# Kernel tuning notes

Measured on AMD Instinct MI355X. Metric: run time of the kernel, lower is better.

Reference implementation:

```python
import jax, jax.numpy as jnp
import numpy as np

D_MODEL = 1024
D_FF = 4096
NUM_EXPERTS = 8
TOP_K = 2
LB_COEF = 0.01
Z_COEF = 0.001
EPS_LN = 1e-5


def setup_inputs() -> dict:
    key = jax.random.key(0)
    ks = jax.random.split(key, 8)
    B, L = 4, 2048
    s_in = 1.0 / np.sqrt(D_MODEL)
    s_ff = 1.0 / np.sqrt(D_FF)
    return {
        "x": jax.random.normal(ks[0], (B, L, D_MODEL), dtype=jnp.float32),
        "gate_w": jax.random.normal(ks[1], (NUM_EXPERTS, D_MODEL), dtype=jnp.float32) * s_in,
        "ln_g": jnp.ones((D_MODEL,), dtype=jnp.float32),
        "ln_b": jnp.zeros((D_MODEL,), dtype=jnp.float32),
        "w1": jax.random.normal(ks[2], (NUM_EXPERTS, D_MODEL, D_FF), dtype=jnp.float32) * s_in,
        "b1": jnp.zeros((NUM_EXPERTS, D_FF), dtype=jnp.float32),
        "w2": jax.random.normal(ks[3], (NUM_EXPERTS, D_FF, D_MODEL), dtype=jnp.float32) * s_ff,
        "b2": jnp.zeros((NUM_EXPERTS, D_MODEL), dtype=jnp.float32),
    }


def reference(x, gate_w, ln_g, ln_b, w1, b1, w2, b2):
    B, L, D = x.shape
    xf = x.reshape(-1, D)  # [T, D]

    # LayerNorm
    mu = jnp.mean(xf, axis=-1, keepdims=True)
    var = jnp.mean((xf - mu) ** 2, axis=-1, keepdims=True)
    x_norm = (xf - mu) * jax.lax.rsqrt(var + EPS_LN) * ln_g + ln_b

    # Router (eval mode: no noise)
    logits = jnp.clip(x_norm @ gate_w.T, -10.0, 10.0)  # [T, E]
    z_loss = jnp.mean(jax.nn.logsumexp(logits, axis=-1) ** 2) * Z_COEF
    probs = jax.nn.softmax(logits, axis=-1)

    gw, idx = jax.lax.top_k(probs, TOP_K)  # [T, K]
    gw = gw / (jnp.sum(gw, axis=-1, keepdims=True) + 1e-8)

    # Load-balancing aux loss uses top-1 assignment
    top1_mask = jax.nn.one_hot(idx[:, 0], NUM_EXPERTS, dtype=jnp.float32)
    fraction_routed = jnp.mean(top1_mask, axis=0)
    mean_prob = jnp.mean(probs, axis=0)
    aux_loss = NUM_EXPERTS * jnp.sum(fraction_routed * mean_prob) * LB_COEF
    total_aux = aux_loss + z_loss

    # Combine weights [T, E]: sum over k of gate weight where routed to e
    combine = jnp.einsum("tk,tke->te", gw, jax.nn.one_hot(idx, NUM_EXPERTS, dtype=gw.dtype))

    # Dense per-expert FFN (Expert: Linear -> GELU -> Linear), combined by weights
    out = jnp.zeros_like(xf)
    for e in range(NUM_EXPERTS):
        h = jax.nn.gelu(x_norm @ w1[e] + b1[e], approximate=False)
        y = h @ w2[e] + b2[e]
        out = out + combine[:, e:e + 1] * y

    return x + out.reshape(B, L, D), total_aux
```

## Files before the change

kernel.cpp:

```cpp
#include <hip/hip_runtime.h>
#include <math.h>

typedef __bf16 bf16_t;
typedef bf16_t bf16x8 __attribute__((ext_vector_type(8)));
typedef bf16_t bf16x4 __attribute__((ext_vector_type(4)));
typedef float  f32x4  __attribute__((ext_vector_type(4)));

#define T_TOK 8192
#define DM 1024
#define DF 4096
#define NE 8
#define NP 16384

__device__ __forceinline__ f32x4 mfma_bf16(bf16x8 a, bf16x8 b, f32x4 c) {
  return __builtin_amdgcn_mfma_f32_16x16x32_bf16(a, b, c, 0, 0, 0);
}

__device__ __forceinline__ void gload16(const void* g, void* l) {
  __builtin_amdgcn_global_load_lds((const __attribute__((address_space(1))) void*)g,
                                   (__attribute__((address_space(3))) void*)l, 16, 0, 0);
}

__device__ __forceinline__ float erf_fast(float x) {
  float ax = fabsf(x);
  float t = 1.f / (1.f + 0.3275911f * ax);
  float p = t * (0.254829592f + t * (-0.284496736f + t * (1.421413741f +
            t * (-1.453152027f + t * 1.061405429f))));
  float r = 1.f - p * __expf(-ax * ax);
  return copysignf(r, x);
}

__device__ __forceinline__ unsigned swz_off(int row, int ch) {
  return (unsigned)(((row >> 1) << 7) + (((((row & 1) << 2) | ch) ^ ((row >> 1) & 7)) << 4));
}


__global__ __launch_bounds__(256) void k_router(
    const float* __restrict__ x, const float* __restrict__ gate_w,
    const float* __restrict__ ln_g, const float* __restrict__ ln_b,
    float* __restrict__ out, bf16_t* __restrict__ xn,
    int* __restrict__ eidx, float* __restrict__ gts, int* __restrict__ meta)
{
  int* cnt1 = meta;
  int* cnt2 = meta + 8;
  float* probsum = (float*)(meta + 32);
  float* zsum    = (float*)(meta + 40);

  __shared__ float sprob[8];
  __shared__ float sz;
  __shared__ int sc1[8], sc2[8];
  if (threadIdx.x < 8) { sprob[threadIdx.x] = 0.f; sc1[threadIdx.x] = 0; sc2[threadIdx.x] = 0; }
  if (threadIdx.x == 8) sz = 0.f;
  __syncthreads();

  int lane = threadIdx.x & 63, wv = threadIdx.x >> 6;
  int t = blockIdx.x * 4 + wv;
  const float* xt = x + (size_t)t * DM;

  float4 v[4];
  float s1 = 0.f, s2 = 0.f;
  #pragma unroll
  for (int c = 0; c < 4; ++c) {
    v[c] = *(const float4*)(xt + c * 256 + lane * 4);
    s1 += v[c].x + v[c].y + v[c].z + v[c].w;
    s2 += v[c].x * v[c].x + v[c].y * v[c].y + v[c].z * v[c].z + v[c].w * v[c].w;
  }
  #pragma unroll
  for (int o = 32; o > 0; o >>= 1) { s1 += __shfl_xor(s1, o, 64); s2 += __shfl_xor(s2, o, 64); }
  float mu = s1 * (1.f / DM);
  float var = s2 * (1.f / DM) - mu * mu;
  float rstd = rsqrtf(var + 1e-5f);

  float xv[16];
  #pragma unroll
  for (int c = 0; c < 4; ++c) {
    int d = c * 256 + lane * 4;
    float4 g4 = *(const float4*)(ln_g + d);
    float4 b4 = *(const float4*)(ln_b + d);
    xv[c*4+0] = (v[c].x - mu) * rstd * g4.x + b4.x;
    xv[c*4+1] = (v[c].y - mu) * rstd * g4.y + b4.y;
    xv[c*4+2] = (v[c].z - mu) * rstd * g4.z + b4.z;
    xv[c*4+3] = (v[c].w - mu) * rstd * g4.w + b4.w;
    *(float4*)(out + (size_t)t * DM + d) = v[c];
    bf16x4 pk = { (bf16_t)xv[c*4+0], (bf16_t)xv[c*4+1], (bf16_t)xv[c*4+2], (bf16_t)xv[c*4+3] };
    *(bf16x4*)(xn + (size_t)t * DM + d) = pk;
  }

  float lg[8];
  #pragma unroll
  for (int e = 0; e < 8; ++e) {
    float p = 0.f;
    #pragma unroll
    for (int c = 0; c < 4; ++c) {
      int d = c * 256 + lane * 4;
      float4 g4 = *(const float4*)(gate_w + e * DM + d);
      p += xv[c*4+0] * g4.x + xv[c*4+1] * g4.y + xv[c*4+2] * g4.z + xv[c*4+3] * g4.w;
    }
    #pragma unroll
    for (int o = 32; o > 0; o >>= 1) p += __shfl_xor(p, o, 64);
    lg[e] = p;
  }

  if (lane == 0) {
    float m = -1e30f;
    #pragma unroll
    for (int e = 0; e < 8; ++e) { lg[e] = fminf(fmaxf(lg[e], -10.f), 10.f); m = fmaxf(m, lg[e]); }
    float pr[8]; float se = 0.f;
    #pragma unroll
    for (int e = 0; e < 8; ++e) { pr[e] = expf(lg[e] - m); se += pr[e]; }
    float inv = 1.f / se;
    #pragma unroll
    for (int e = 0; e < 8; ++e) pr[e] *= inv;
    float lse = m + logf(se);

    int e0 = 0; float p0 = pr[0];
    #pragma unroll
    for (int e = 1; e < 8; ++e) if (pr[e] > p0) { p0 = pr[e]; e0 = e; }
    int e1 = -1; float p1 = -1.f;
    #pragma unroll
    for (int e = 0; e < 8; ++e) if (e != e0 && pr[e] > p1) { p1 = pr[e]; e1 = e; }
    float s = p0 + p1 + 1e-8f;
    eidx[t*2]   = e0; eidx[t*2+1] = e1;
    gts[t*2]    = p0 / s; gts[t*2+1] = p1 / s;

    atomicAdd(&sc1[e0], 1);
    atomicAdd(&sc2[e0], 1);
    atomicAdd(&sc2[e1], 1);
    #pragma unroll
    for (int e = 0; e < 8; ++e) atomicAdd(&sprob[e], pr[e]);
    atomicAdd(&sz, lse * lse);
  }
  __syncthreads();
  if (threadIdx.x < 8) {
    if (sc1[threadIdx.x]) atomicAdd(&cnt1[threadIdx.x], sc1[threadIdx.x]);
    if (sc2[threadIdx.x]) atomicAdd(&cnt2[threadIdx.x], sc2[threadIdx.x]);
    atomicAdd(&probsum[threadIdx.x], sprob[threadIdx.x]);
  }
  if (threadIdx.x == 8) atomicAdd(zsum, sz);
}

__global__ __launch_bounds__(256) void k_convT2(
    const float* __restrict__ w1, bf16_t* __restrict__ w1t,
    const float* __restrict__ w2, bf16_t* __restrict__ w2t)
{
  int bid = blockIdx.x;
  const float* s; bf16_t* d; int R, C, c0, r0;
  if (bid < 8192) {
    int e = bid >> 10, rem = bid & 1023;
    R = DM; C = DF;
    s = w1 + (size_t)e * R * C; d = w1t + (size_t)e * R * C;
    c0 = (rem & 63) * 64; r0 = (rem >> 6) * 64;
  } else {
    int e = (bid - 8192) >> 10, rem = (bid - 8192) & 1023;
    R = DF; C = DM;
    s = w2 + (size_t)e * R * C; d = w2t + (size_t)e * R * C;
    c0 = (rem & 15) * 64; r0 = (rem >> 4) * 64;
  }

  __shared__ float tile[64][65];
  int t = threadIdx.x;
  #pragma unroll
  for (int i = 0; i < 4; ++i) {
    int idx = i * 256 + t;
    int r = idx >> 4, c4 = (idx & 15) * 4;
    float4 v = *(const float4*)(s + (size_t)(r0 + r) * C + c0 + c4);
    tile[r][c4]   = v.x; tile[r][c4+1] = v.y;
    tile[r][c4+2] = v.z; tile[r][c4+3] = v.w;
  }
  __syncthreads();
  #pragma unroll
  for (int i = 0; i < 2; ++i) {
    int idx = i * 256 + t;
    int c = idx >> 3, r8 = (idx & 7) * 8;
    bf16x8 pk;
    #pragma unroll
    for (int k = 0; k < 8; ++k) pk[k] = (bf16_t)tile[r8 + k][c];
    *(bf16x8*)(d + (size_t)(c0 + c) * R + r0 + r8) = pk;
  }
}

__global__ void k_finalize(int* __restrict__ meta, float* __restrict__ aux_out) {
  if (threadIdx.x == 0 && blockIdx.x == 0) {
    int acc = 0;
    for (int e = 0; e < 8; ++e) { meta[24 + e] = acc; acc += meta[8 + e]; }
    const float* probsum = (const float*)(meta + 32);
    const float* zsum    = (const float*)(meta + 40);
    float s = 0.f;
    for (int e = 0; e < 8; ++e)
      s += ((float)meta[e] * (1.f / 8192.f)) * (probsum[e] * (1.f / 8192.f));
    aux_out[0] = 8.f * s * 0.01f + (zsum[0] * (1.f / 8192.f)) * 0.001f;
  }
}

__global__ __launch_bounds__(256) void k_assign(
    const int* __restrict__ eidx, float* __restrict__ gts,
    int* __restrict__ meta, int* __restrict__ list, float* __restrict__ gl,
    int* __restrict__ t2s)
{
  int t = blockIdx.x * 256 + threadIdx.x;
  int* cursor = meta + 16;
  const int* off = meta + 24;
  #pragma unroll
  for (int k = 0; k < 2; ++k) {
    int e = eidx[t*2 + k];
    float g = gts[t*2 + k];
    int pos = atomicAdd(&cursor[e], 1);
    int slot = off[e] + pos;
    list[slot] = t;
    gl[slot] = g;
    t2s[t*2 + k] = slot;
  }
}


#define STAGE1(KT, BO) do { \
  _Pragma("unroll") for (int r = 0; r < 2; ++r) gload16(sA[r] + (KT) * 32, smem + (BO) + dA[r]); \
  _Pragma("unroll") for (int r = 0; r < 4; ++r) gload16(sB[r] + (KT) * 32, smem + (BO) + dB[r]); \
} while (0)

#define COMPUTE1(BO) do { \
  bf16x8 bfr[4]; \
  _Pragma("unroll") for (int j = 0; j < 4; ++j) bfr[j] = *(const bf16x8*)(smem + (BO) + b_off[j]); \
  _Pragma("unroll") for (int i = 0; i < 8; ++i) { \
    bf16x8 af = *(const bf16x8*)(smem + (BO) + a_off[i]); \
    _Pragma("unroll") for (int j = 0; j < 4; ++j) acc[i][j] = mfma_bf16(af, bfr[j], acc[i][j]); \
  } \
} while (0)

#define WAITV6 do { __builtin_amdgcn_sched_barrier(0); \
  asm volatile("s_waitcnt vmcnt(6)" ::: "memory"); \
  __builtin_amdgcn_sched_barrier(0); __builtin_amdgcn_s_barrier(); \
  __builtin_amdgcn_sched_barrier(0); } while (0)

#define WAITV0 do { __builtin_amdgcn_sched_barrier(0); \
  asm volatile("s_waitcnt vmcnt(0)" ::: "memory"); \
  __builtin_amdgcn_sched_barrier(0); __builtin_amdgcn_s_barrier(); \
  __builtin_amdgcn_sched_barrier(0); } while (0)

#define ENDBAR do { __builtin_amdgcn_sched_barrier(0); \
  __builtin_amdgcn_s_barrier(); __builtin_amdgcn_sched_barrier(0); } while (0)

#define KLOOP(NT) do { \
  STAGE1(0, 0); \
  for (int kt = 0; kt < (NT); kt += 2) { \
    STAGE1(kt + 1, 24576); \
    WAITV6; \
    __builtin_amdgcn_s_setprio(1); \
    COMPUTE1(0); \
    __builtin_amdgcn_s_setprio(0); \
    ENDBAR; \
    if (kt + 2 < (NT)) { STAGE1(kt + 2, 0); WAITV6; } else { WAITV0; } \
    __builtin_amdgcn_s_setprio(1); \
    COMPUTE1(24576); \
    __builtin_amdgcn_s_setprio(0); \
    ENDBAR; \
  } \
} while (0)

__global__ __launch_bounds__(256, 2) void k_ffn1(
    const bf16_t* __restrict__ xn, const bf16_t* __restrict__ w1t,
    const float* __restrict__ b1, bf16_t* __restrict__ H,
    const int* __restrict__ list, const int* __restrict__ meta)
{
  int e = blockIdx.z;
  int cnt = meta[8 + e];
  int m0 = blockIdx.y * 128;
  if (m0 >= cnt) return;
  int offe = meta[24 + e];
  int n0 = blockIdx.x * 256;

  __shared__ __align__(1024) char smem[49152];
  int tid = threadIdx.x, lane = tid & 63, wv = tid >> 6;

  const bf16_t* sA[2]; const bf16_t* sB[4];
  unsigned dA[2], dB[4];
  #pragma unroll
  for (int i = 0; i < 2; ++i) {
    int s = i * 256 + tid;
    int line = s >> 3, u = s & 7, w = u ^ (line & 7);
    int row = (line << 1) | (w >> 2), ch = w & 3;
    int mrow = min(m0 + row, cnt - 1);
    int token = list[offe + mrow];
    sA[i] = xn + (size_t)token * DM + ch * 8;
    dA[i] = (unsigned)(i * 4096 + wv * 1024);
  }
  #pragma unroll
  for (int i = 0; i < 4; ++i) {
    int s = i * 256 + tid;
    int line = s >> 3, u = s & 7, w = u ^ (line & 7);
    int row = (line << 1) | (w >> 2), ch = w & 3;
    sB[i] = w1t + ((size_t)e * DF + n0 + row) * DM + ch * 8;
    dB[i] = (unsigned)(8192 + i * 4096 + wv * 1024);
  }

  unsigned a_off[8], b_off[4];
  #pragma unroll
  for (int i = 0; i < 8; ++i) a_off[i] = swz_off(i * 16 + (lane & 15), lane >> 4);
  #pragma unroll
  for (int j = 0; j < 4; ++j) b_off[j] = 8192u + swz_off(wv * 64 + j * 16 + (lane & 15), lane >> 4);

  f32x4 acc[8][4];
  #pragma unroll
  for (int i = 0; i < 8; ++i)
    #pragma unroll
    for (int j = 0; j < 4; ++j)
      acc[i][j] = (f32x4){0.f, 0.f, 0.f, 0.f};

  KLOOP(DM / 32);

  int rq = (lane >> 4) << 2;
  int cbase = n0 + wv * 64 + (lane & 15);
  #pragma unroll
  for (int i = 0; i < 8; ++i) {
    #pragma unroll
    for (int q = 0; q < 4; ++q) {
      int mg = m0 + i * 16 + rq + q;
      if (mg < cnt) {
        size_t hrow = (size_t)(offe + mg) * DF;
        #pragma unroll
        for (int j = 0; j < 4; ++j) {
          int col = cbase + j * 16;
          float hv = acc[i][j][q] + b1[e * DF + col];
          hv = 0.5f * hv * (1.f + erf_fast(hv * 0.70710678118f));
          H[hrow + col] = (bf16_t)hv;
        }
      }
    }
  }
}

__global__ __launch_bounds__(256, 2) void k_ffn2(
    const bf16_t* __restrict__ H, const bf16_t* __restrict__ w2t,
    const float* __restrict__ b2, bf16_t* __restrict__ Y,
    const int* __restrict__ meta)
{
  int e = blockIdx.z;
  int cnt = meta[8 + e];
  int m0 = blockIdx.y * 128;
  if (m0 >= cnt) return;
  int offe = meta[24 + e];
  int n0 = blockIdx.x * 256;

  __shared__ __align__(1024) char smem[49152];
  int tid = threadIdx.x, lane = tid & 63, wv = tid >> 6;

  const bf16_t* sA[2]; const bf16_t* sB[4];
  unsigned dA[2], dB[4];
  #pragma unroll
  for (int i = 0; i < 2; ++i) {
    int s = i * 256 + tid;
    int line = s >> 3, u = s & 7, w = u ^ (line & 7);
    int row = (line << 1) | (w >> 2), ch = w & 3;
    int mrow = min(m0 + row, cnt - 1);
    sA[i] = H + (size_t)(offe + mrow) * DF + ch * 8;
    dA[i] = (unsigned)(i * 4096 + wv * 1024);
  }
  #pragma unroll
  for (int i = 0; i < 4; ++i) {
    int s = i * 256 + tid;
    int line = s >> 3, u = s & 7, w = u ^ (line & 7);
    int row = (line << 1) | (w >> 2), ch = w & 3;
    sB[i] = w2t + ((size_t)e * DM + n0 + row) * DF + ch * 8;
    dB[i] = (unsigned)(8192 + i * 4096 + wv * 1024);
  }

  unsigned a_off[8], b_off[4];
  #pragma unroll
  for (int i = 0; i < 8; ++i) a_off[i] = swz_off(i * 16 + (lane & 15), lane >> 4);
  #pragma unroll
  for (int j = 0; j < 4; ++j) b_off[j] = 8192u + swz_off(wv * 64 + j * 16 + (lane & 15), lane >> 4);

  f32x4 acc[8][4];
  #pragma unroll
  for (int i = 0; i < 8; ++i)
    #pragma unroll
    for (int j = 0; j < 4; ++j)
      acc[i][j] = (f32x4){0.f, 0.f, 0.f, 0.f};

  KLOOP(DF / 32);

  int rq = (lane >> 4) << 2;
  int cbase = n0 + wv * 64 + (lane & 15);
  #pragma unroll
  for (int i = 0; i < 8; ++i) {
    #pragma unroll
    for (int q = 0; q < 4; ++q) {
      int mg = m0 + i * 16 + rq + q;
      if (mg < cnt) {
        size_t yrow = (size_t)(offe + mg) * DM;
        #pragma unroll
        for (int j = 0; j < 4; ++j) {
          int col = cbase + j * 16;
          Y[yrow + col] = (bf16_t)(acc[i][j][q] + b2[e * DM + col]);
        }
      }
    }
  }
}

__global__ __launch_bounds__(256) void k_combine(
    const bf16_t* __restrict__ Y, const int* __restrict__ t2s,
    const float* __restrict__ gl, float* __restrict__ out)
{
  int lane = threadIdx.x & 63, wv = threadIdx.x >> 6;
  int t = blockIdx.x * 4 + wv;
  int s0 = t2s[t*2], s1 = t2s[t*2 + 1];
  float g0 = gl[s0], g1 = gl[s1];
  const bf16_t* y0 = Y + (size_t)s0 * DM;
  const bf16_t* y1 = Y + (size_t)s1 * DM;
  float* o = out + (size_t)t * DM;
  #pragma unroll
  for (int c = 0; c < 4; ++c) {
    int d = c * 256 + lane * 4;
    float4 r  = *(const float4*)(o + d);
    bf16x4 a = *(const bf16x4*)(y0 + d);
    bf16x4 b = *(const bf16x4*)(y1 + d);
    r.x += g0 * (float)a[0] + g1 * (float)b[0];
    r.y += g0 * (float)a[1] + g1 * (float)b[1];
    r.z += g0 * (float)a[2] + g1 * (float)b[2];
    r.w += g0 * (float)a[3] + g1 * (float)b[3];
    *(float4*)(o + d) = r;
  }
}

extern "C" void kernel_launch(void* const* d_in, const int* in_sizes, int n_in,
                              void* d_out, int out_size, void* d_ws, size_t ws_size,
                              hipStream_t stream) {
  const float* x      = (const float*)d_in[0];
  const float* gate_w = (const float*)d_in[1];
  const float* ln_g   = (const float*)d_in[2];
  const float* ln_b   = (const float*)d_in[3];
  const float* w1     = (const float*)d_in[4];
  const float* b1     = (const float*)d_in[5];
  const float* w2     = (const float*)d_in[6];
  const float* b2     = (const float*)d_in[7];
  float* out = (float*)d_out;

  char* ws = (char*)d_ws;
  bf16_t* xn   = (bf16_t*)(ws);
  bf16_t* w1t  = (bf16_t*)(ws + 16777216ull);
  bf16_t* Y    = (bf16_t*)(ws + 16777216ull);
  bf16_t* w2t  = (bf16_t*)(ws + 83886080ull);
  bf16_t* H    = (bf16_t*)(ws + 150994944ull);
  int*    list = (int*)   (ws + 285212672ull);
  float*  gl   = (float*) (ws + 285278208ull);
  int*    eidx = (int*)   (ws + 285343744ull);
  float*  gts  = (float*) (ws + 285409280ull);
  int*    t2s  = (int*)   (ws + 285409280ull);
  int*    meta = (int*)   (ws + 285474816ull);

  hipMemsetAsync(meta, 0, 256, stream);
  k_router<<<T_TOK / 4, 256, 0, stream>>>(x, gate_w, ln_g, ln_b, out, xn, eidx, gts, meta);
  k_convT2<<<16384, 256, 0, stream>>>(w1, w1t, w2, w2t);
  k_finalize<<<1, 1, 0, stream>>>(meta, out + (size_t)T_TOK * DM);
  k_assign<<<T_TOK / 256, 256, 0, stream>>>(eidx, gts, meta, list, gl, t2s);
  k_ffn1<<<dim3(DF / 256, 64, NE), 256, 0, stream>>>(xn, w1t, b1, H, list, meta);
  k_ffn2<<<dim3(DM / 256, 64, NE), 256, 0, stream>>>(H, w2t, b2, Y, meta);
  k_combine<<<T_TOK / 4, 256, 0, stream>>>(Y, t2s, gl, out);
}
```

Measured before the change: 685.5 us.

## Use 256x256 tiles with 8 waves and a deeper LDS-pipelined GEMM

Both expert FFN GEMMs switch from 128x256 tiles with 4 waves to 256x256 tiles with 8 waves (a 2x4 wave grid). They use 128KB of dynamic LDS holding two buffers of BK=64 split into 32-wide halves. The k-loop is rewritten so global-to-LDS loads for future tiles are interleaved with half-tile MFMA phases, with finer waits and barriers. The aim is better operand reuse per loaded byte and more latency hiding. In exchange, occupancy drops to one block per CU, the grid has fewer blocks, and there are more barriers.

```diff
diff --git a/kernel.cpp b/kernel.cpp
--- a/kernel.cpp
+++ b/kernel.cpp
@@ -213,91 +213,91 @@
 }
 
 
-#define STAGE1(KT, BO) do { \
-  _Pragma("unroll") for (int r = 0; r < 2; ++r) gload16(sA[r] + (KT) * 32, smem + (BO) + dA[r]); \
-  _Pragma("unroll") for (int r = 0; r < 4; ++r) gload16(sB[r] + (KT) * 32, smem + (BO) + dB[r]); \
+#define PBAR do { __builtin_amdgcn_sched_barrier(0); __builtin_amdgcn_s_barrier(); \
+                  __builtin_amdgcn_sched_barrier(0); } while (0)
+#define VWAIT10 do { __builtin_amdgcn_sched_barrier(0); \
+  asm volatile("s_waitcnt vmcnt(10)" ::: "memory"); \
+  __builtin_amdgcn_sched_barrier(0); } while (0)
+#define VWAIT0 do { __builtin_amdgcn_sched_barrier(0); \
+  asm volatile("s_waitcnt vmcnt(0)" ::: "memory"); \
+  __builtin_amdgcn_sched_barrier(0); } while (0)
+
+#define STG_A(T, KS, P) do { \
+  gload16(sAq[0] + (T)*64 + (KS)*32, smem + (P)*65536 + (KS)*16384 + dq[0]); \
+  gload16(sAq[1] + (T)*64 + (KS)*32, smem + (P)*65536 + (KS)*16384 + dq[1]); } while (0)
+#define STG_B(T, KS, P) do { \
+  gload16(sBq[0] + (T)*64 + (KS)*32, smem + (P)*65536 + 32768 + (KS)*16384 + dq[0]); \
+  gload16(sBq[1] + (T)*64 + (KS)*32, smem + (P)*65536 + 32768 + (KS)*16384 + dq[1]); } while (0)
+#define LDA(P, KS) do { _Pragma("unroll") for (int i_ = 0; i_ < 8; ++i_) \
+  afr[i_] = *(const bf16x8*)(smem + (P)*65536 + (KS)*16384 + a_off[i_]); } while (0)
+#define LDB(P, KS, NH) do { \
+  bfr0 = *(const bf16x8*)(smem + (P)*65536 + 32768 + (KS)*16384 + b_off[(NH)*2+0]); \
+  bfr1 = *(const bf16x8*)(smem + (P)*65536 + 32768 + (KS)*16384 + b_off[(NH)*2+1]); } while (0)
+#define FMA(NH) do { __builtin_amdgcn_s_setprio(1); \
+  _Pragma("unroll") for (int i_ = 0; i_ < 8; ++i_) { \
+    acc[i_][(NH)*2+0] = mfma_bf16(afr[i_], bfr0, acc[i_][(NH)*2+0]); \
+    acc[i_][(NH)*2+1] = mfma_bf16(afr[i_], bfr1, acc[i_][(NH)*2+1]); } \
+  __builtin_amdgcn_s_setprio(0); } while (0)
+
+#define TILE_MAIN(T, P) do { \
+  LDA(P,0); LDB(P,0,0); STG_B((T)+1, 1, (P)^1); PBAR; FMA(0); PBAR; \
+  LDB(P,0,1); STG_A((T)+2, 0, P); VWAIT10; PBAR; FMA(1); PBAR; \
+  LDA(P,1); LDB(P,1,0); STG_B((T)+2, 0, P); PBAR; FMA(0); PBAR; \
+  LDB(P,1,1); STG_A((T)+2, 1, P); VWAIT10; PBAR; FMA(1); PBAR; } while (0)
+
+#define GEMM_PIPE(NT) do { \
+  STG_A(0,0,0); STG_B(0,0,0); STG_A(0,1,0); STG_B(0,1,0); \
+  STG_A(1,0,1); STG_B(1,0,1); STG_A(1,1,1); \
+  VWAIT10; PBAR; \
+  for (int t_ = 0; t_ < (NT) - 2; t_ += 2) { TILE_MAIN(t_, 0); TILE_MAIN(t_ + 1, 1); } \
+   \
+  LDA(0,0); LDB(0,0,0); STG_B((NT)-1, 1, 1); PBAR; FMA(0); PBAR; \
+  LDB(0,0,1); VWAIT0; PBAR; FMA(1); PBAR; \
+  LDA(0,1); LDB(0,1,0); PBAR; FMA(0); PBAR; \
+  LDB(0,1,1); PBAR; FMA(1); PBAR; \
+   \
+  LDA(1,0); LDB(1,0,0); PBAR; FMA(0); PBAR; \
+  LDB(1,0,1); PBAR; FMA(1); PBAR; \
+  LDA(1,1); LDB(1,1,0); PBAR; FMA(0); PBAR; \
+  LDB(1,1,1); PBAR; FMA(1); \
 } while (0)
 
-#define COMPUTE1(BO) do { \
-  bf16x8 bfr[4]; \
-  _Pragma("unroll") for (int j = 0; j < 4; ++j) bfr[j] = *(const bf16x8*)(smem + (BO) + b_off[j]); \
-  _Pragma("unroll") for (int i = 0; i < 8; ++i) { \
-    bf16x8 af = *(const bf16x8*)(smem + (BO) + a_off[i]); \
-    _Pragma("unroll") for (int j = 0; j < 4; ++j) acc[i][j] = mfma_bf16(af, bfr[j], acc[i][j]); \
-  } \
-} while (0)
-
-#define WAITV6 do { __builtin_amdgcn_sched_barrier(0); \
-  asm volatile("s_waitcnt vmcnt(6)" ::: "memory"); \
-  __builtin_amdgcn_sched_barrier(0); __builtin_amdgcn_s_barrier(); \
-  __builtin_amdgcn_sched_barrier(0); } while (0)
-
-#define WAITV0 do { __builtin_amdgcn_sched_barrier(0); \
-  asm volatile("s_waitcnt vmcnt(0)" ::: "memory"); \
-  __builtin_amdgcn_sched_barrier(0); __builtin_amdgcn_s_barrier(); \
-  __builtin_amdgcn_sched_barrier(0); } while (0)
-
-#define ENDBAR do { __builtin_amdgcn_sched_barrier(0); \
-  __builtin_amdgcn_s_barrier(); __builtin_amdgcn_sched_barrier(0); } while (0)
-
-#define KLOOP(NT) do { \
-  STAGE1(0, 0); \
-  for (int kt = 0; kt < (NT); kt += 2) { \
-    STAGE1(kt + 1, 24576); \
-    WAITV6; \
-    __builtin_amdgcn_s_setprio(1); \
-    COMPUTE1(0); \
-    __builtin_amdgcn_s_setprio(0); \
-    ENDBAR; \
-    if (kt + 2 < (NT)) { STAGE1(kt + 2, 0); WAITV6; } else { WAITV0; } \
-    __builtin_amdgcn_s_setprio(1); \
-    COMPUTE1(24576); \
-    __builtin_amdgcn_s_setprio(0); \
-    ENDBAR; \
-  } \
-} while (0)
-
-__global__ __launch_bounds__(256, 2) void k_ffn1(
+__global__ __launch_bounds__(512, 1) void k_ffn1(
     const bf16_t* __restrict__ xn, const bf16_t* __restrict__ w1t,
     const float* __restrict__ b1, bf16_t* __restrict__ H,
     const int* __restrict__ list, const int* __restrict__ meta)
 {
+  extern __shared__ char smem[];
   int e = blockIdx.z;
   int cnt = meta[8 + e];
-  int m0 = blockIdx.y * 128;
+  int m0 = blockIdx.y * 256;
   if (m0 >= cnt) return;
   int offe = meta[24 + e];
   int n0 = blockIdx.x * 256;
 
-  __shared__ __align__(1024) char smem[49152];
   int tid = threadIdx.x, lane = tid & 63, wv = tid >> 6;
-
-  const bf16_t* sA[2]; const bf16_t* sB[4];
-  unsigned dA[2], dB[4];
+  int wm = wv >> 2, wn = wv & 3;
+
+  const bf16_t* sAq[2]; const bf16_t* sBq[2];
+  unsigned dq[2];
   #pragma unroll
   for (int i = 0; i < 2; ++i) {
-    int s = i * 256 + tid;
+    int s = i * 512 + tid;
     int line = s >> 3, u = s & 7, w = u ^ (line & 7);
     int row = (line << 1) | (w >> 2), ch = w & 3;
     int mrow = min(m0 + row, cnt - 1);
     int token = list[offe + mrow];
-    sA[i] = xn + (size_t)token * DM + ch * 8;
-    dA[i] = (unsigned)(i * 4096 + wv * 1024);
-  }
-  #pragma unroll
-  for (int i = 0; i < 4; ++i) {
-    int s = i * 256 + tid;
-    int line = s >> 3, u = s & 7, w = u ^ (line & 7);
-    int row = (line << 1) | (w >> 2), ch = w & 3;
-    sB[i] = w1t + ((size_t)e * DF + n0 + row) * DM + ch * 8;
-    dB[i] = (unsigned)(8192 + i * 4096 + wv * 1024);
+    sAq[i] = xn + (size_t)token * DM + ch * 8;
+    sBq[i] = w1t + ((size_t)e * DF + n0 + row) * DM + ch * 8;
+    dq[i] = (unsigned)(i * 8192 + wv * 1024);
   }
 
   unsigned a_off[8], b_off[4];
   #pragma unroll
-  for (int i = 0; i < 8; ++i) a_off[i] = swz_off(i * 16 + (lane & 15), lane >> 4);
-  #pragma unroll
-  for (int j = 0; j < 4; ++j) b_off[j] = 8192u + swz_off(wv * 64 + j * 16 + (lane & 15), lane >> 4);
+  for (int i = 0; i < 8; ++i) a_off[i] = swz_off(wm * 128 + i * 16 + (lane & 15), lane >> 4);
+  #pragma unroll
+  for (int j = 0; j < 4; ++j)
+    b_off[j] = swz_off(wn * 64 + (j >> 1) * 32 + (j & 1) * 16 + (lane & 15), lane >> 4);
 
   f32x4 acc[8][4];
   #pragma unroll
@@ -305,21 +305,22 @@
     #pragma unroll
     for (int j = 0; j < 4; ++j)
       acc[i][j] = (f32x4){0.f, 0.f, 0.f, 0.f};
-
-  KLOOP(DM / 32);
+  bf16x8 afr[8], bfr0, bfr1;
+
+  GEMM_PIPE(DM / 64);
 
   int rq = (lane >> 4) << 2;
-  int cbase = n0 + wv * 64 + (lane & 15);
+  int cb = n0 + wn * 64 + (lane & 15);
   #pragma unroll
   for (int i = 0; i < 8; ++i) {
     #pragma unroll
     for (int q = 0; q < 4; ++q) {
-      int mg = m0 + i * 16 + rq + q;
+      int mg = m0 + wm * 128 + i * 16 + rq + q;
       if (mg < cnt) {
         size_t hrow = (size_t)(offe + mg) * DF;
         #pragma unroll
         for (int j = 0; j < 4; ++j) {
-          int col = cbase + j * 16;
+          int col = cb + (j >> 1) * 32 + (j & 1) * 16;
           float hv = acc[i][j][q] + b1[e * DF + col];
           hv = 0.5f * hv * (1.f + erf_fast(hv * 0.70710678118f));
           H[hrow + col] = (bf16_t)hv;
@@ -329,46 +330,41 @@
   }
 }
 
-__global__ __launch_bounds__(256, 2) void k_ffn2(
+__global__ __launch_bounds__(512, 1) void k_ffn2(
     const bf16_t* __restrict__ H, const bf16_t* __restrict__ w2t,
     const float* __restrict__ b2, bf16_t* __restrict__ Y,
     const int* __restrict__ meta)
 {
+  extern __shared__ char smem[];
   int e = blockIdx.z;
   int cnt = meta[8 + e];
-  int m0 = blockIdx.y * 128;
+  int m0 = blockIdx.y * 256;
   if (m0 >= cnt) return;
   int offe = meta[24 + e];
   int n0 = blockIdx.x * 256;
 
-  __shared__ __align__(1024) char smem[49152];
   int tid = threadIdx.x, lane = tid & 63, wv = tid >> 6;
-
-  const bf16_t* sA[2]; const bf16_t* sB[4];
-  unsigned dA[2], dB[4];
+  int wm = wv >> 2, wn = wv & 3;
+
+  const bf16_t* sAq[2]; const bf16_t* sBq[2];
+  unsigned dq[2];
   #pragma unroll
   for (int i = 0; i < 2; ++i) {
-    int s = i * 256 + tid;
+    int s = i * 512 + tid;
     int line = s >> 3, u = s & 7, w = u ^ (line & 7);
     int row = (line << 1) | (w >> 2), ch = w & 3;
     int mrow = min(m0 + row, cnt - 1);
-    sA[i] = H + (size_t)(offe + mrow) * DF + ch * 8;
-    dA[i] = (unsigned)(i * 4096 + wv * 1024);
-  }
-  #pragma unroll
-  for (int i = 0; i < 4; ++i) {
-    int s = i * 256 + tid;
-    int line = s >> 3, u = s & 7, w = u ^ (line & 7);
-    int row = (line << 1) | (w >> 2), ch = w & 3;
-    sB[i] = w2t + ((size_t)e * DM + n0 + row) * DF + ch * 8;
-    dB[i] = (unsigned)(8192 + i * 4096 + wv * 1024);
+    sAq[i] = H + (size_t)(offe + mrow) * DF + ch * 8;
+    sBq[i] = w2t + ((size_t)e * DM + n0 + row) * DF + ch * 8;
+    dq[i] = (unsigned)(i * 8192 + wv * 1024);
   }
 
   unsigned a_off[8], b_off[4];
   #pragma unroll
-  for (int i = 0; i < 8; ++i) a_off[i] = swz_off(i * 16 + (lane & 15), lane >> 4);
-  #pragma unroll
-  for (int j = 0; j < 4; ++j) b_off[j] = 8192u + swz_off(wv * 64 + j * 16 + (lane & 15), lane >> 4);
+  for (int i = 0; i < 8; ++i) a_off[i] = swz_off(wm * 128 + i * 16 + (lane & 15), lane >> 4);
+  #pragma unroll
+  for (int j = 0; j < 4; ++j)
+    b_off[j] = swz_off(wn * 64 + (j >> 1) * 32 + (j & 1) * 16 + (lane & 15), lane >> 4);
 
   f32x4 acc[8][4];
   #pragma unroll
@@ -376,21 +372,22 @@
     #pragma unroll
     for (int j = 0; j < 4; ++j)
       acc[i][j] = (f32x4){0.f, 0.f, 0.f, 0.f};
-
-  KLOOP(DF / 32);
+  bf16x8 afr[8], bfr0, bfr1;
+
+  GEMM_PIPE(DF / 64);
 
   int rq = (lane >> 4) << 2;
-  int cbase = n0 + wv * 64 + (lane & 15);
+  int cb = n0 + wn * 64 + (lane & 15);
   #pragma unroll
   for (int i = 0; i < 8; ++i) {
     #pragma unroll
     for (int q = 0; q < 4; ++q) {
-      int mg = m0 + i * 16 + rq + q;
+      int mg = m0 + wm * 128 + i * 16 + rq + q;
       if (mg < cnt) {
         size_t yrow = (size_t)(offe + mg) * DM;
         #pragma unroll
         for (int j = 0; j < 4; ++j) {
-          int col = cbase + j * 16;
+          int col = cb + (j >> 1) * 32 + (j & 1) * 16;
           Y[yrow + col] = (bf16_t)(acc[i][j][q] + b2[e * DM + col]);
         }
       }
@@ -449,12 +446,15 @@
   int*    t2s  = (int*)   (ws + 285409280ull);
   int*    meta = (int*)   (ws + 285474816ull);
 
+  hipFuncSetAttribute((const void*)k_ffn1, hipFuncAttributeMaxDynamicSharedMemorySize, 131072);
+  hipFuncSetAttribute((const void*)k_ffn2, hipFuncAttributeMaxDynamicSharedMemorySize, 131072);
+
   hipMemsetAsync(meta, 0, 256, stream);
   k_router<<<T_TOK / 4, 256, 0, stream>>>(x, gate_w, ln_g, ln_b, out, xn, eidx, gts, meta);
   k_convT2<<<16384, 256, 0, stream>>>(w1, w1t, w2, w2t);
   k_finalize<<<1, 1, 0, stream>>>(meta, out + (size_t)T_TOK * DM);
   k_assign<<<T_TOK / 256, 256, 0, stream>>>(eidx, gts, meta, list, gl, t2s);
-  k_ffn1<<<dim3(DF / 256, 64, NE), 256, 0, stream>>>(xn, w1t, b1, H, list, meta);
-  k_ffn2<<<dim3(DM / 256, 64, NE), 256, 0, stream>>>(H, w2t, b2, Y, meta);
+  k_ffn1<<<dim3(DF / 256, 32, NE), 512, 131072, stream>>>(xn, w1t, b1, H, list, meta);
+  k_ffn2<<<dim3(DM / 256, 32, NE), 512, 131072, stream>>>(H, w2t, b2, Y, meta);
   k_combine<<<T_TOK / 4, 256, 0, stream>>>(Y, t2s, gl, out);
 }
```

Result: faster. 663.1 us (-3.3%).

## Split GEMM tile across 8 waves with 2x4 wave grid in FFN kernels

Applied to the files above, without the earlier changes.

The FFN GEMM kernels move from 256 threads (4 waves, each computing 128x64) to 512 threads (8 waves in a 2x4 grid, each computing 64x64). Each thread now issues three 16-byte global-to-LDS loads per stage instead of six, and the vmcnt wait is adjusted to match. Halving the per-wave accumulator count lowers register pressure and is meant to raise occupancy and latency hiding. In exchange, each wave gets less MFMA work per LDS fragment load and the larger workgroup synchronises more waves at every barrier.

```diff
diff --git a/kernel.cpp b/kernel.cpp
--- a/kernel.cpp
+++ b/kernel.cpp
@@ -213,55 +213,42 @@
 }
 
 
-#define STAGE1(KT, BO) do { \
-  _Pragma("unroll") for (int r = 0; r < 2; ++r) gload16(sA[r] + (KT) * 32, smem + (BO) + dA[r]); \
-  _Pragma("unroll") for (int r = 0; r < 4; ++r) gload16(sB[r] + (KT) * 32, smem + (BO) + dB[r]); \
-} while (0)
-
-#define COMPUTE1(BO) do { \
-  bf16x8 bfr[4]; \
-  _Pragma("unroll") for (int j = 0; j < 4; ++j) bfr[j] = *(const bf16x8*)(smem + (BO) + b_off[j]); \
-  _Pragma("unroll") for (int i = 0; i < 8; ++i) { \
-    bf16x8 af = *(const bf16x8*)(smem + (BO) + a_off[i]); \
-    _Pragma("unroll") for (int j = 0; j < 4; ++j) acc[i][j] = mfma_bf16(af, bfr[j], acc[i][j]); \
+#define BAR __builtin_amdgcn_s_barrier()
+#define VW(N) asm volatile("s_waitcnt vmcnt(" #N ")" ::: "memory")
+
+#define STG(T, P) do { \
+  gload16(sA  + (size_t)(T) * 32, smem + (P) * 24576 +         wv * 1024); \
+  gload16(sB0 + (size_t)(T) * 32, smem + (P) * 24576 +  8192 + wv * 1024); \
+  gload16(sB1 + (size_t)(T) * 32, smem + (P) * 24576 + 16384 + wv * 1024); } while (0)
+
+#define COMP(P) do { \
+  bf16x8 afr[4], bfr[4]; \
+  _Pragma("unroll") for (int i_ = 0; i_ < 4; ++i_) \
+    afr[i_] = *(const bf16x8*)(smem + (P) * 24576 + a_off[i_]); \
+  _Pragma("unroll") for (int j_ = 0; j_ < 4; ++j_) \
+    bfr[j_] = *(const bf16x8*)(smem + (P) * 24576 + 8192 + b_off[j_]); \
+  __builtin_amdgcn_s_setprio(1); \
+  _Pragma("unroll") for (int i_ = 0; i_ < 4; ++i_) \
+    _Pragma("unroll") for (int j_ = 0; j_ < 4; ++j_) \
+      acc[i_][j_] = mfma_bf16(afr[i_], bfr[j_], acc[i_][j_]); \
+  __builtin_amdgcn_s_setprio(0); } while (0)
+
+#define KLOOP(NT) do { \
+  STG(0, 0); \
+  for (int kt = 0; kt < (NT); kt += 2) { \
+    if (kt + 1 < (NT)) { STG(kt + 1, 1); VW(3); } else { VW(0); } \
+    BAR; COMP(0); BAR; \
+    if (kt + 2 < (NT)) { STG(kt + 2, 0); VW(3); } else { VW(0); } \
+    BAR; COMP(1); BAR; \
   } \
 } while (0)
 
-#define WAITV6 do { __builtin_amdgcn_sched_barrier(0); \
-  asm volatile("s_waitcnt vmcnt(6)" ::: "memory"); \
-  __builtin_amdgcn_sched_barrier(0); __builtin_amdgcn_s_barrier(); \
-  __builtin_amdgcn_sched_barrier(0); } while (0)
-
-#define WAITV0 do { __builtin_amdgcn_sched_barrier(0); \
-  asm volatile("s_waitcnt vmcnt(0)" ::: "memory"); \
-  __builtin_amdgcn_sched_barrier(0); __builtin_amdgcn_s_barrier(); \
-  __builtin_amdgcn_sched_barrier(0); } while (0)
-
-#define ENDBAR do { __builtin_amdgcn_sched_barrier(0); \
-  __builtin_amdgcn_s_barrier(); __builtin_amdgcn_sched_barrier(0); } while (0)
-
-#define KLOOP(NT) do { \
-  STAGE1(0, 0); \
-  for (int kt = 0; kt < (NT); kt += 2) { \
-    STAGE1(kt + 1, 24576); \
-    WAITV6; \
-    __builtin_amdgcn_s_setprio(1); \
-    COMPUTE1(0); \
-    __builtin_amdgcn_s_setprio(0); \
-    ENDBAR; \
-    if (kt + 2 < (NT)) { STAGE1(kt + 2, 0); WAITV6; } else { WAITV0; } \
-    __builtin_amdgcn_s_setprio(1); \
-    COMPUTE1(24576); \
-    __builtin_amdgcn_s_setprio(0); \
-    ENDBAR; \
-  } \
-} while (0)
-
-__global__ __launch_bounds__(256, 2) void k_ffn1(
+__global__ __launch_bounds__(512, 4) void k_ffn1(
     const bf16_t* __restrict__ xn, const bf16_t* __restrict__ w1t,
     const float* __restrict__ b1, bf16_t* __restrict__ H,
     const int* __restrict__ list, const int* __restrict__ meta)
 {
+  __shared__ __align__(1024) char smem[49152];
   int e = blockIdx.z;
   int cnt = meta[8 + e];
   int m0 = blockIdx.y * 128;
@@ -269,52 +256,50 @@
   int offe = meta[24 + e];
   int n0 = blockIdx.x * 256;
 
-  __shared__ __align__(1024) char smem[49152];
   int tid = threadIdx.x, lane = tid & 63, wv = tid >> 6;
-
-  const bf16_t* sA[2]; const bf16_t* sB[4];
-  unsigned dA[2], dB[4];
-  #pragma unroll
-  for (int i = 0; i < 2; ++i) {
-    int s = i * 256 + tid;
-    int line = s >> 3, u = s & 7, w = u ^ (line & 7);
+  int wm = wv >> 2, wn = wv & 3;
+
+  const bf16_t* sA; const bf16_t* sB0; const bf16_t* sB1;
+  {
+    int s = tid, line = s >> 3, u = s & 7, w = u ^ (line & 7);
     int row = (line << 1) | (w >> 2), ch = w & 3;
     int mrow = min(m0 + row, cnt - 1);
     int token = list[offe + mrow];
-    sA[i] = xn + (size_t)token * DM + ch * 8;
-    dA[i] = (unsigned)(i * 4096 + wv * 1024);
-  }
-  #pragma unroll
-  for (int i = 0; i < 4; ++i) {
-    int s = i * 256 + tid;
-    int line = s >> 3, u = s & 7, w = u ^ (line & 7);
-    int row = (line << 1) | (w >> 2), ch = w & 3;
-    sB[i] = w1t + ((size_t)e * DF + n0 + row) * DM + ch * 8;
-    dB[i] = (unsigned)(8192 + i * 4096 + wv * 1024);
-  }
-
-  unsigned a_off[8], b_off[4];
-  #pragma unroll
-  for (int i = 0; i < 8; ++i) a_off[i] = swz_off(i * 16 + (lane & 15), lane >> 4);
-  #pragma unroll
-  for (int j = 0; j < 4; ++j) b_off[j] = 8192u + swz_off(wv * 64 + j * 16 + (lane & 15), lane >> 4);
-
-  f32x4 acc[8][4];
-  #pragma unroll
-  for (int i = 0; i < 8; ++i)
+    sA = xn + (size_t)token * DM + ch * 8;
+  }
+  {
+    int s = tid, line = s >> 3, u = s & 7, w = u ^ (line & 7);
+    int row = (line << 1) | (w >> 2), ch = w & 3;
+    sB0 = w1t + ((size_t)e * DF + n0 + row) * DM + ch * 8;
+  }
+  {
+    int s = 512 + tid, line = s >> 3, u = s & 7, w = u ^ (line & 7);
+    int row = (line << 1) | (w >> 2), ch = w & 3;
+    sB1 = w1t + ((size_t)e * DF + n0 + row) * DM + ch * 8;
+  }
+
+  unsigned a_off[4], b_off[4];
+  #pragma unroll
+  for (int i = 0; i < 4; ++i) a_off[i] = swz_off(wm * 64 + i * 16 + (lane & 15), lane >> 4);
+  #pragma unroll
+  for (int j = 0; j < 4; ++j) b_off[j] = swz_off(wn * 64 + j * 16 + (lane & 15), lane >> 4);
+
+  f32x4 acc[4][4];
+  #pragma unroll
+  for (int i = 0; i < 4; ++i)
     #pragma unroll
     for (int j = 0; j < 4; ++j)
       acc[i][j] = (f32x4){0.f, 0.f, 0.f, 0.f};
 
   KLOOP(DM / 32);
 
-  int rq = (lane >> 4) << 2;
-  int cbase = n0 + wv * 64 + (lane & 15);
-  #pragma unroll
-  for (int i = 0; i < 8; ++i) {
+  int rbase = wm * 64 + ((lane >> 4) << 2);
+  int cbase = n0 + wn * 64 + (lane & 15);
+  #pragma unroll
+  for (int i = 0; i < 4; ++i) {
     #pragma unroll
     for (int q = 0; q < 4; ++q) {
-      int mg = m0 + i * 16 + rq + q;
+      int mg = m0 + rbase + i * 16 + q;
       if (mg < cnt) {
         size_t hrow = (size_t)(offe + mg) * DF;
         #pragma unroll
@@ -329,11 +314,12 @@
   }
 }
 
-__global__ __launch_bounds__(256, 2) void k_ffn2(
+__global__ __launch_bounds__(512, 4) void k_ffn2(
     const bf16_t* __restrict__ H, const bf16_t* __restrict__ w2t,
     const float* __restrict__ b2, bf16_t* __restrict__ Y,
     const int* __restrict__ meta)
 {
+  __shared__ __align__(1024) char smem[49152];
   int e = blockIdx.z;
   int cnt = meta[8 + e];
   int m0 = blockIdx.y * 128;
@@ -341,51 +327,49 @@
   int offe = meta[24 + e];
   int n0 = blockIdx.x * 256;
 
-  __shared__ __align__(1024) char smem[49152];
   int tid = threadIdx.x, lane = tid & 63, wv = tid >> 6;
-
-  const bf16_t* sA[2]; const bf16_t* sB[4];
-  unsigned dA[2], dB[4];
-  #pragma unroll
-  for (int i = 0; i < 2; ++i) {
-    int s = i * 256 + tid;
-    int line = s >> 3, u = s & 7, w = u ^ (line & 7);
+  int wm = wv >> 2, wn = wv & 3;
+
+  const bf16_t* sA; const bf16_t* sB0; const bf16_t* sB1;
+  {
+    int s = tid, line = s >> 3, u = s & 7, w = u ^ (line & 7);
     int row = (line << 1) | (w >> 2), ch = w & 3;
     int mrow = min(m0 + row, cnt - 1);
-    sA[i] = H + (size_t)(offe + mrow) * DF + ch * 8;
-    dA[i] = (unsigned)(i * 4096 + wv * 1024);
-  }
-  #pragma unroll
-  for (int i = 0; i < 4; ++i) {
-    int s = i * 256 + tid;
-    int line = s >> 3, u = s & 7, w = u ^ (line & 7);
-    int row = (line << 1) | (w >> 2), ch = w & 3;
-    sB[i] = w2t + ((size_t)e * DM + n0 + row) * DF + ch * 8;
-    dB[i] = (unsigned)(8192 + i * 4096 + wv * 1024);
-  }
-
-  unsigned a_off[8], b_off[4];
-  #pragma unroll
-  for (int i = 0; i < 8; ++i) a_off[i] = swz_off(i * 16 + (lane & 15), lane >> 4);
-  #pragma unroll
-  for (int j = 0; j < 4; ++j) b_off[j] = 8192u + swz_off(wv * 64 + j * 16 + (lane & 15), lane >> 4);
-
-  f32x4 acc[8][4];
-  #pragma unroll
-  for (int i = 0; i < 8; ++i)
+    sA = H + (size_t)(offe + mrow) * DF + ch * 8;
+  }
+  {
+    int s = tid, line = s >> 3, u = s & 7, w = u ^ (line & 7);
+    int row = (line << 1) | (w >> 2), ch = w & 3;
+    sB0 = w2t + ((size_t)e * DM + n0 + row) * DF + ch * 8;
+  }
+  {
+    int s = 512 + tid, line = s >> 3, u = s & 7, w = u ^ (line & 7);
+    int row = (line << 1) | (w >> 2), ch = w & 3;
+    sB1 = w2t + ((size_t)e * DM + n0 + row) * DF + ch * 8;
+  }
+
+  unsigned a_off[4], b_off[4];
+  #pragma unroll
+  for (int i = 0; i < 4; ++i) a_off[i] = swz_off(wm * 64 + i * 16 + (lane & 15), lane >> 4);
+  #pragma unroll
+  for (int j = 0; j < 4; ++j) b_off[j] = swz_off(wn * 64 + j * 16 + (lane & 15), lane >> 4);
+
+  f32x4 acc[4][4];
+  #pragma unroll
+  for (int i = 0; i < 4; ++i)
     #pragma unroll
     for (int j = 0; j < 4; ++j)
       acc[i][j] = (f32x4){0.f, 0.f, 0.f, 0.f};
 
   KLOOP(DF / 32);
 
-  int rq = (lane >> 4) << 2;
-  int cbase = n0 + wv * 64 + (lane & 15);
-  #pragma unroll
-  for (int i = 0; i < 8; ++i) {
+  int rbase = wm * 64 + ((lane >> 4) << 2);
+  int cbase = n0 + wn * 64 + (lane & 15);
+  #pragma unroll
+  for (int i = 0; i < 4; ++i) {
     #pragma unroll
     for (int q = 0; q < 4; ++q) {
-      int mg = m0 + i * 16 + rq + q;
+      int mg = m0 + rbase + i * 16 + q;
       if (mg < cnt) {
         size_t yrow = (size_t)(offe + mg) * DM;
         #pragma unroll
@@ -454,7 +438,7 @@
   k_convT2<<<16384, 256, 0, stream>>>(w1, w1t, w2, w2t);
   k_finalize<<<1, 1, 0, stream>>>(meta, out + (size_t)T_TOK * DM);
   k_assign<<<T_TOK / 256, 256, 0, stream>>>(eidx, gts, meta, list, gl, t2s);
-  k_ffn1<<<dim3(DF / 256, 64, NE), 256, 0, stream>>>(xn, w1t, b1, H, list, meta);
-  k_ffn2<<<dim3(DM / 256, 64, NE), 256, 0, stream>>>(H, w2t, b2, Y, meta);
+  k_ffn1<<<dim3(DF / 256, 64, NE), 512, 0, stream>>>(xn, w1t, b1, H, list, meta);
+  k_ffn2<<<dim3(DM / 256, 64, NE), 512, 0, stream>>>(H, w2t, b2, Y, meta);
   k_combine<<<T_TOK / 4, 256, 0, stream>>>(Y, t2s, gl, out);
 }
```

Result: faster. 667.4 us (-2.6%).
